# Optimization experiments

Measured on AMD Instinct MI355X. Metric: run time of the kernel, lower is better.

The kernel has to match this reference:

```python
import jax, jax.numpy as jnp
import numpy as np

B, S, L = 512, 150, 50          # batch, history length, prediction horizon
D, H, FF, NL = 128, 8, 256, 2   # d_model, heads, ffn hidden, encoder layers
DT = 0.1                        # self.dt


def _layernorm(x, g, b, eps=1e-5):
    mu = jnp.mean(x, axis=-1, keepdims=True)
    var = jnp.mean((x - mu) ** 2, axis=-1, keepdims=True)
    return (x - mu) / jnp.sqrt(var + eps) * g + b


def setup_inputs() -> dict:
    key = jax.random.key(0)
    ks = jax.random.split(key, 16)
    # inputs[:, :, :] = (position y, speed v, gap s, delta_v) over history
    pos = 100.0 * jax.random.uniform(ks[0], (B, S), jnp.float32)
    vel = 5.0 + 20.0 * jax.random.uniform(ks[1], (B, S), jnp.float32)
    gap = 10.0 + 30.0 * jax.random.uniform(ks[2], (B, S), jnp.float32)
    dvel = 0.5 * jax.random.normal(ks[3], (B, S), jnp.float32)
    inputs = jnp.stack([pos, vel, gap, dvel], axis=-1)
    # his_labels: leader position / speed over the horizon; keep leader ahead
    lead_y = inputs[:, -1, 0:1] + inputs[:, -1, 2:3] + 15.0 * jnp.arange(1, L + 1, dtype=jnp.float32)[None, :]
    lead_v = 15.0 + 2.0 * jax.random.uniform(ks[4], (B, L), jnp.float32)
    his_labels = jnp.stack([lead_y, lead_v], axis=-1)

    def u(k, shape, scale=0.05):
        return scale * jax.random.normal(k, shape, jnp.float32)

    params = dict(
        emb_w=u(ks[5], (D, 1)), emb_b=jnp.zeros((D,), jnp.float32),
        ipw=u(ks[6], (NL, 3 * D, D)), ipb=jnp.zeros((NL, 3 * D), jnp.float32),
        opw=u(ks[7], (NL, D, D)), opb=jnp.zeros((NL, D), jnp.float32),
        ln1g=jnp.ones((NL, D), jnp.float32), ln1b=jnp.zeros((NL, D), jnp.float32),
        l1w=u(ks[8], (NL, FF, D)), l1b=jnp.zeros((NL, FF), jnp.float32),
        l2w=u(ks[9], (NL, D, FF)), l2b=jnp.zeros((NL, D), jnp.float32),
        ln2g=jnp.ones((NL, D), jnp.float32), ln2b=jnp.zeros((NL, D), jnp.float32),
        dec_w=u(ks[10], (1, D)), dec_b=jnp.zeros((1,), jnp.float32),
        fus_w=u(ks[11], (1, 3)), fus_b=jnp.zeros((1,), jnp.float32),
    )
    return dict(inputs=inputs, his_labels=his_labels,
                s_0_input=jnp.float32(2.0), T_input=jnp.float32(1.5),
                a_input=jnp.float32(1.0), b_input=jnp.float32(1.5),
                v_d_input=jnp.float32(30.0), **params)


def _encoder_layer(x, mask, ipw, ipb, opw, opb, ln1g, ln1b, l1w, l1b, l2w, l2b, ln2g, ln2b):
    # x: [S, B, D]; torch post-norm TransformerEncoderLayer, relu, dropout=0
    Sq, Bb, Dd = x.shape
    dh = Dd // H
    qkv = x @ ipw.T + ipb                       # [S, B, 3D]
    q, k, v = jnp.split(qkv, 3, axis=-1)

    def heads(t):                               # [S, B, D] -> [B, H, S, dh]
        return t.reshape(Sq, Bb, H, dh).transpose(1, 2, 0, 3)

    q, k, v = heads(q), heads(k), heads(v)
    scores = jnp.einsum('bhqd,bhkd->bhqk', q, k) / jnp.sqrt(jnp.float32(dh)) + mask
    attn = jax.nn.softmax(scores, axis=-1)
    o = jnp.einsum('bhqk,bhkd->bhqd', attn, v).transpose(2, 0, 1, 3).reshape(Sq, Bb, Dd)
    o = o @ opw.T + opb
    x = _layernorm(x + o, ln1g, ln1b)
    ff = jax.nn.relu(x @ l1w.T + l1b) @ l2w.T + l2b
    return _layernorm(x + ff, ln2g, ln2b)


def _idm(inp_last, his, s0, T, a, b, vd, dt):
    # inp_last: [B, 4] = (y, v, s, delta_v); his: [B, L, 2] leader (y, v)
    y, v, s, dv = inp_last[:, 0], inp_last[:, 1], inp_last[:, 2], inp_last[:, 3]
    sq = 2.0 * jnp.sqrt(a * b)
    s_x = s0 + jnp.maximum(0.0, v * T + v * dv / sq)
    a_f = a * (1.0 - (v / vd) ** 4 - (s_x / s) ** 2)
    v0 = jnp.maximum(v + a_f * dt, 0.0)
    # NOTE: faithful to the torch source's bug: after the clipping loop the
    # loop variable i == B-1, so y_pred[:,0,0] = y + v_pred[B-1,0,0]*dt uses
    # the LAST batch element's speed for every row.
    y0 = y + v0[-1] * dt

    def step(carry, his_j):
        vj, yj = carry
        dvj = his_j[:, 1] - vj
        sj = his_j[:, 0] - yj
        sx = s0 + jnp.maximum(0.0, vj * T + vj * dvj / sq)
        acc = a * (1.0 - (vj / vd) ** 4 - (sx / sj) ** 2)
        v2 = vj + acc * dt
        v2 = jnp.where(v2 <= 0.0, 0.0, v2)
        y2 = yj + v2 * dt
        return (v2, y2), y2

    _, ys = jax.lax.scan(step, (v0, y0), his[:, :L - 1].transpose(1, 0, 2))  # ys: [L-1, B]
    y_pred = jnp.concatenate([y0[:, None], ys.T], axis=1)  # [B, L]
    return y_pred[:, :, None]


def reference(inputs, his_labels, s_0_input, T_input, a_input, b_input, v_d_input,
              emb_w, emb_b, ipw, ipb, opw, opb, ln1g, ln1b,
              l1w, l1b, l2w, l2b, ln2g, ln2b, dec_w, dec_b, fus_w, fus_b):
    src_in = inputs[:, :, 0:1]                               # [B, S, 1]
    src = src_in.transpose(1, 0, 2) @ emb_w.T + emb_b       # [S, B, D]
    mask = jnp.where(jnp.tril(jnp.ones((S, S), bool)), 0.0, -jnp.inf).astype(src.dtype)
    x = src
    for l in range(NL):
        x = _encoder_layer(x, mask, ipw[l], ipb[l], opw[l], opb[l],
                           ln1g[l], ln1b[l], l1w[l], l1b[l],
                           l2w[l], l2b[l], ln2g[l], ln2b[l])
    enc = x[-1]                                              # [B, D]
    out = jnp.broadcast_to(enc, (L, B, D)) @ dec_w.T + dec_b  # [L, B, 1]
    out = out.transpose(1, 0, 2)                             # [B, L, 1]
    # hist: per-row linspace(last, last + dv*L, L+1)[1:] == last + dv*(1..L)
    last = src_in[:, -1, 0]
    dvh = (last - src_in[:, -(1 + L), 0]) / L
    hist = (last[:, None] + dvh[:, None] * jnp.arange(1, L + 1, dtype=last.dtype))[:, :, None]
    y_idm = _idm(inputs[:, -1, :], his_labels, s_0_input, T_input,
                 a_input, b_input, v_d_input, DT)
    fusion = jnp.concatenate([out, hist, y_idm], axis=2)     # [B, L, 3]
    return fusion @ fus_w.T + fus_b                          # [B, L, 1]
```

## Files before the change

kernel.cpp:

```cpp
#include <hip/hip_runtime.h>

#define BB   512
#define SS   150
#define LL   50
#define DD   128
#define HH   8
#define DHH  16
#define FFD  256
#define NLL  2
#define MM   (SS*BB)
#define MDSZ ((size_t)MM*DD)
#define MLAST 76288

typedef unsigned short u16;
typedef __attribute__((ext_vector_type(8))) short short8;
typedef __attribute__((ext_vector_type(4))) float f32x4;

__device__ __forceinline__ float bf2f(u16 u) {
    return __uint_as_float(((unsigned int)u) << 16);
}
__device__ __forceinline__ u16 f2bf(float f) {
    unsigned int x = __float_as_uint(f);
    unsigned int r = (x + 0x7fffu + ((x >> 16) & 1u)) >> 16;
    return (u16)r;
}
__device__ __forceinline__ float ldv(const void* p, size_t i, int bf) {
    return bf ? bf2f(((const u16*)p)[i]) : ((const float*)p)[i];
}
__device__ __forceinline__ float rd_scalar(const void* p) {
    const u16* q = (const u16*)p;
    u16 lo = q[0];
    if (lo != 0) return bf2f(lo);
    return *(const float*)p;
}
__device__ __forceinline__ f32x4 mfma16(short8 a, short8 b, f32x4 c) {
    return __builtin_amdgcn_mfma_f32_16x16x32_bf16(a, b, c, 0, 0, 0);
}
__device__ __forceinline__ float fexp2(float x) {
#if __has_builtin(__builtin_amdgcn_exp2f)
    return __builtin_amdgcn_exp2f(x);
#else
    return exp2f(x);
#endif
}
__device__ __forceinline__ float frcp(float x) {
#if __has_builtin(__builtin_amdgcn_rcpf)
    return __builtin_amdgcn_rcpf(x);
#else
    return 1.f / x;
#endif
}

__global__ void detect_kernel(const u16* __restrict__ ln1g, int* __restrict__ flag)
{
    *flag = (ln1g[0] == 0x3F80) ? 1 : 0;
}

#define WOFF_IPW 0
#define WOFF_OPW 98304
#define WOFF_L1W 131072
#define WOFF_L2W 196608
#define WTOTAL   262144
__global__ __launch_bounds__(256) void prep_kernel(
    const void* __restrict__ ipw, const void* __restrict__ opw,
    const void* __restrict__ l1w, const void* __restrict__ l2w,
    u16* __restrict__ wbf, const int* __restrict__ flag)
{
    int bf = *flag;
    int idx = blockIdx.x * 256 + threadIdx.x;
    if (idx >= WTOTAL) return;
    const void* src; size_t i;
    if (idx < WOFF_OPW)      { src = ipw; i = idx; }
    else if (idx < WOFF_L1W) { src = opw; i = idx - WOFF_OPW; }
    else if (idx < WOFF_L2W) { src = l1w; i = idx - WOFF_L1W; }
    else                     { src = l2w; i = idx - WOFF_L2W; }
    wbf[idx] = bf ? ((const u16*)src)[i] : f2bf(((const float*)src)[i]);
}

__global__ void prep2_kernel(
    const void* __restrict__ ipw, const void* __restrict__ ipb,
    const void* __restrict__ emb_w, const void* __restrict__ emb_b,
    float* __restrict__ uw, const int* __restrict__ flag)
{
    int bf = *flag;
    int c = threadIdx.x;
    float su = 0.f, sw = 0.f;
    for (int k = 0; k < DD; ++k) {
        float wv = ldv(ipw, (size_t)c * DD + k, bf);
        su += wv * ldv(emb_w, k, bf);
        sw += wv * ldv(emb_b, k, bf);
    }
    uw[c]       = su;
    uw[384 + c] = sw + ldv(ipb, c, bf);
}

__global__ __launch_bounds__(192) void attn0_kernel(
    const void* __restrict__ inputs, const float* __restrict__ uw,
    u16* __restrict__ o, const int* __restrict__ flag)
{
    __shared__ float pos_s[SS];
    __shared__ float pmax_s[SS];
    __shared__ float pmin_s[SS];

    int bid = blockIdx.x;
    int h = bid & 7, b = bid >> 3;
    int tid = threadIdx.x;
    int bf = *flag;

    if (tid < SS) pos_s[tid] = ldv(inputs, (size_t)(b * SS + tid) * 4 + 0, bf);
    __syncthreads();
    if (tid == 0) {
        float mx = pos_s[0], mn = pos_s[0];
        pmax_s[0] = mx; pmin_s[0] = mn;
        for (int t = 1; t < SS; ++t) {
            mx = fmaxf(mx, pos_s[t]); mn = fminf(mn, pos_s[t]);
            pmax_s[t] = mx; pmin_s[t] = mn;
        }
    }

    const float* uq = uw + h * 16;
    const float* wq = uw + 384 + h * 16;
    const float* uk = uw + 128 + h * 16;
    float A = 0.f, Bc = 0.f;
#pragma unroll
    for (int d = 0; d < 16; ++d) { A += uq[d] * uk[d]; Bc += wq[d] * uk[d]; }
    __syncthreads();

    int q = tid;
    if (q >= SS) return;
    float pq  = pos_s[q];
    const float L2E = 1.4426950408889634f;
    float cql = 0.25f * (pq * A + Bc) * L2E;
    float Ml  = fmaxf(cql * pmax_s[q], cql * pmin_s[q]);
    float s = 0.f, wsum = 0.f;
    for (int t = 0; t <= q; ++t) {
        float pt = pos_s[t];
        float e = fexp2(__builtin_fmaf(cql, pt, -Ml));
        s += e; wsum += e * pt;
    }
    float mq = wsum * frcp(s);

    const float* uv = uw + 256 + h * 16;
    const float* wv = uw + 384 + 256 + h * 16;
    u16 ov[16];
#pragma unroll
    for (int d = 0; d < 16; ++d) ov[d] = f2bf(mq * uv[d] + wv[d]);
    u16* dst = o + ((size_t)q * BB + b) * DD + h * DHH;
    *(uint4*)(dst)     = *(uint4*)(ov);
    *(uint4*)(dst + 8) = *(uint4*)(ov + 8);
}

#define LDPK 72
template<int EPI>
__global__ __launch_bounds__(256) void mfma_gemm(
    const u16* __restrict__ A, const u16* __restrict__ W,
    const void* __restrict__ bias, size_t boff,
    void* __restrict__ out, const u16* __restrict__ resid,
    int N, int K, const int* __restrict__ flag,
    const void* __restrict__ lng, const void* __restrict__ lnb, size_t goff,
    const void* __restrict__ ew, const void* __restrict__ eb)
{
    __shared__ __attribute__((aligned(16))) u16 As[64 * LDPK];
    __shared__ __attribute__((aligned(16))) u16 Bs[128 * LDPK];

    int bf = *flag;
    int tid  = threadIdx.x;
    int wave = tid >> 6, lane = tid & 63;
    int wy = wave >> 1, wx = wave & 1;
    int quad = lane >> 4, lr = lane & 15;
    int m0 = blockIdx.x * 64, n0 = blockIdx.y * 128;

    int aR = tid >> 2,          aC = (tid & 3) * 16;
    int bR0 = tid >> 2,         bC0 = (tid & 3) * 16;
    int bR1 = (tid + 256) >> 2, bC1 = (tid & 3) * 16;

    f32x4 acc[2][4] = {};

    for (int k0 = 0; k0 < K; k0 += 64) {
        const u16* ap  = A + (size_t)(m0 + aR) * K + k0 + aC;
        const u16* wp0 = W + (size_t)(n0 + bR0) * K + k0 + bC0;
        const u16* wp1 = W + (size_t)(n0 + bR1) * K + k0 + bC1;
        uint4 av0 = *(const uint4*)(ap);
        uint4 av1 = *(const uint4*)(ap + 8);
        uint4 w00 = *(const uint4*)(wp0);
        uint4 w01 = *(const uint4*)(wp0 + 8);
        uint4 w10 = *(const uint4*)(wp1);
        uint4 w11 = *(const uint4*)(wp1 + 8);
        __syncthreads();
        *(uint4*)(As + aR * LDPK + aC)       = av0;
        *(uint4*)(As + aR * LDPK + aC + 8)   = av1;
        *(uint4*)(Bs + bR0 * LDPK + bC0)     = w00;
        *(uint4*)(Bs + bR0 * LDPK + bC0 + 8) = w01;
        *(uint4*)(Bs + bR1 * LDPK + bC1)     = w10;
        *(uint4*)(Bs + bR1 * LDPK + bC1 + 8) = w11;
        __syncthreads();

#pragma unroll
        for (int ks = 0; ks < 64; ks += 32) {
            short8 a[2], b[4];
#pragma unroll
            for (int i = 0; i < 2; ++i)
                a[i] = *(const short8*)(As + (wy * 32 + i * 16 + lr) * LDPK + ks + quad * 8);
#pragma unroll
            for (int j = 0; j < 4; ++j)
                b[j] = *(const short8*)(Bs + (wx * 64 + j * 16 + lr) * LDPK + ks + quad * 8);
#pragma unroll
            for (int i = 0; i < 2; ++i)
#pragma unroll
                for (int j = 0; j < 4; ++j)
                    acc[i][j] = mfma16(a[i], b[j], acc[i][j]);
        }
    }

    if (EPI == 3 || EPI == 4) {
        float bvj[4];
#pragma unroll
        for (int j = 0; j < 4; ++j) bvj[j] = ldv(bias, boff + wx * 64 + j * 16 + lr, bf);

        float ewj[4], ebj[4], posr[2][4];
        if (EPI == 4) {
            int sblk  = m0 >> 9;
            int bbase = m0 & 511;
#pragma unroll
            for (int j = 0; j < 4; ++j) {
                int c = wx * 64 + j * 16 + lr;
                ewj[j] = ldv(ew, c, bf);
                ebj[j] = ldv(eb, c, bf);
            }
#pragma unroll
            for (int i = 0; i < 2; ++i)
#pragma unroll
                for (int r = 0; r < 4; ++r) {
                    int b = bbase + wy * 32 + i * 16 + quad * 4 + r;
                    posr[i][r] = ldv((const void*)resid, (size_t)(b * SS + sblk) * 4 + 0, bf);
                }
        }

        float s1[2][4] = {}, s2[2][4] = {};
#pragma unroll
        for (int j = 0; j < 4; ++j) {
            int c = wx * 64 + j * 16 + lr;
#pragma unroll
            for (int i = 0; i < 2; ++i)
#pragma unroll
                for (int r = 0; r < 4; ++r) {
                    int m = m0 + wy * 32 + i * 16 + quad * 4 + r;
                    float rv = (EPI == 4)
                               ? __builtin_fmaf(posr[i][r], ewj[j], ebj[j])
                               : bf2f(resid[(size_t)m * 128 + c]);
                    float v = acc[i][j][r] + bvj[j] + rv;
                    acc[i][j][r] = v;
                    s1[i][r] += v;
                    s2[i][r] += v * v;
                }
        }
#pragma unroll
        for (int i = 0; i < 2; ++i)
#pragma unroll
            for (int r = 0; r < 4; ++r)
#pragma unroll
                for (int msk = 1; msk < 16; msk <<= 1) {
                    s1[i][r] += __shfl_xor(s1[i][r], msk);
                    s2[i][r] += __shfl_xor(s2[i][r], msk);
                }

        __syncthreads();
        float* red = (float*)As;
        if (lr == 0) {
#pragma unroll
            for (int i = 0; i < 2; ++i)
#pragma unroll
                for (int r = 0; r < 4; ++r) {
                    int row = wy * 32 + i * 16 + quad * 4 + r;
                    red[wx * 128 + row]      = s1[i][r];
                    red[wx * 128 + 64 + row] = s2[i][r];
                }
        }
        __syncthreads();

        float gj[4], bj[4];
#pragma unroll
        for (int j = 0; j < 4; ++j) {
            int c = wx * 64 + j * 16 + lr;
            gj[j] = ldv(lng, goff + c, bf);
            bj[j] = ldv(lnb, goff + c, bf);
        }
#pragma unroll
        for (int i = 0; i < 2; ++i)
#pragma unroll
            for (int r = 0; r < 4; ++r) {
                int row = wy * 32 + i * 16 + quad * 4 + r;
                float t1 = red[row] + red[128 + row];
                float t2 = red[64 + row] + red[192 + row];
                float mu = t1 * (1.f / 128.f);
                float rstd = rsqrtf(t2 * (1.f / 128.f) - mu * mu + 1e-5f);
                size_t m = (size_t)(m0 + row);
#pragma unroll
                for (int j = 0; j < 4; ++j) {
                    int c = wx * 64 + j * 16 + lr;
                    ((u16*)out)[m * 128 + c] =
                        f2bf((acc[i][j][r] - mu) * rstd * gj[j] + bj[j]);
                }
            }
        return;
    }

#pragma unroll
    for (int j = 0; j < 4; ++j) {
        int c = n0 + wx * 64 + j * 16 + lr;
        float bvj = ldv(bias, boff + c, bf);
#pragma unroll
        for (int i = 0; i < 2; ++i) {
#pragma unroll
            for (int r = 0; r < 4; ++r) {
                int m = m0 + wy * 32 + i * 16 + quad * 4 + r;
                float v = acc[i][j][r] + bvj;
                if (EPI == 1) v = fmaxf(v, 0.f);
                ((u16*)out)[(size_t)m * N + c] = f2bf(v);
            }
        }
    }
}

__global__ __launch_bounds__(256) void attn1_kernel(
    const u16* __restrict__ bx, const u16* __restrict__ w1,
    const void* __restrict__ ipb, u16* __restrict__ o1, const int* __restrict__ flag)
{
    __shared__ __attribute__((aligned(16))) u16 X[SS * 128];
    __shared__ float qv[128];
    __shared__ float qt[8][132];
    __shared__ float cb_s[8];
    __shared__ float E[SS][8];
    __shared__ float ssum[8];

    int bf = *flag;
    int b = blockIdx.x;
    int tid = threadIdx.x;

    for (int idx = tid; idx < SS * 16; idx += 256) {
        int row = idx >> 4, ch = idx & 15;
        *(uint4*)(X + row * 128 + ch * 8) =
            *(const uint4*)(bx + ((size_t)(row * 512 + b)) * 128 + ch * 8);
    }
    __syncthreads();

    if (tid < 128) {
        const u16* wr = w1 + (size_t)tid * 128;
        float acc = 0.f;
        for (int kc = 0; kc < 16; ++kc) {
            short8 wv = *(const short8*)(wr + kc * 8);
            short8 xv = *(const short8*)(X + 149 * 128 + kc * 8);
#pragma unroll
            for (int i = 0; i < 8; ++i)
                acc = __builtin_fmaf(bf2f((u16)wv[i]), bf2f((u16)xv[i]), acc);
        }
        qv[tid] = acc + ldv(ipb, 384 + tid, bf);
    }
    __syncthreads();

    for (int o = tid; o < 1024; o += 256) {
        int h = o >> 7, k = o & 127;
        float acc = 0.f;
#pragma unroll
        for (int d = 0; d < 16; ++d)
            acc = __builtin_fmaf(bf2f(w1[(size_t)(128 + h * 16 + d) * 128 + k]),
                                 qv[h * 16 + d], acc);
        qt[h][k] = acc;
    }
    if (tid < 8) {
        float acc = 0.f;
#pragma unroll
        for (int d = 0; d < 16; ++d)
            acc = __builtin_fmaf(qv[tid * 16 + d],
                                 ldv(ipb, 384 + 128 + tid * 16 + d, bf), acc);
        cb_s[tid] = acc;
    }
    __syncthreads();

    const float Cs = 0.36067376022224085f;
    for (int o = tid; o < SS * 8; o += 256) {
        int t = o >> 3, h = o & 7;
        float acc = 0.f;
        for (int kc = 0; kc < 16; ++kc) {
            short8 xv = *(const short8*)(X + t * 128 + kc * 8);
#pragma unroll
            for (int i = 0; i < 8; ++i)
                acc = __builtin_fmaf(qt[h][kc * 8 + i], bf2f((u16)xv[i]), acc);
        }
        E[t][h] = fexp2((acc + cb_s[h]) * Cs);
    }
    __syncthreads();

    if (tid < 128) {
        int h = tid >> 4, j = tid & 15;
        float acc = 0.f;
        for (int t = j; t < SS; t += 16) acc += E[t][h];
#pragma unroll
        for (int m = 1; m < 16; m <<= 1) acc += __shfl_xor(acc, m);
        if (j == 0) ssum[h] = acc;
    }
    __syncthreads();

    if (tid < 128) {
        int h = tid >> 4, k0 = (tid & 15) * 8;
        float wacc[8] = {};
        for (int t = 0; t < SS; ++t) {
            float e = E[t][h];
            short8 xv = *(const short8*)(X + t * 128 + k0);
#pragma unroll
            for (int i = 0; i < 8; ++i)
                wacc[i] = __builtin_fmaf(e, bf2f((u16)xv[i]), wacc[i]);
        }
#pragma unroll
        for (int i = 0; i < 8; ++i) qt[h][k0 + i] = wacc[i];
    }
    __syncthreads();

    if (tid < 128) {
        int h = tid >> 4;
        const u16* wr = w1 + (size_t)(256 + tid) * 128;
        float acc = 0.f;
        for (int kc = 0; kc < 16; ++kc) {
            short8 wv = *(const short8*)(wr + kc * 8);
#pragma unroll
            for (int i = 0; i < 8; ++i)
                acc = __builtin_fmaf(bf2f((u16)wv[i]), qt[h][kc * 8 + i], acc);
        }
        o1[(size_t)b * 128 + tid] =
            f2bf(acc * frcp(ssum[tid >> 4]) + ldv(ipb, 384 + 256 + tid, bf));
    }
}

__global__ __launch_bounds__(64) void head_kernel(
    const u16* __restrict__ xlast, const void* __restrict__ inputs,
    const void* __restrict__ his,
    const void* s0p, const void* Tp, const void* ap, const void* bp, const void* vdp,
    const void* __restrict__ dec_w, const void* dec_b,
    const void* fus_w, const void* fus_b,
    void* __restrict__ out, const int* __restrict__ flag)
{
    int bf = *flag;
    int b = blockIdx.x * 64 + threadIdx.x;
    if (b >= BB) return;

    const u16* enc = xlast + (size_t)b * DD;
    float dot = 0.f;
    for (int d = 0; d < DD; ++d) dot += bf2f(enc[d]) * ldv(dec_w, d, bf);
    float outv = dot + ldv(dec_b, 0, bf);

    float last = ldv(inputs, (size_t)(b * SS + (SS - 1)) * 4 + 0, bf);
    float prev = ldv(inputs, (size_t)(b * SS + (SS - 1 - LL)) * 4 + 0, bf);
    float dvh = (last - prev) * (1.f / (float)LL);

    float s0 = rd_scalar(s0p), T = rd_scalar(Tp), a = rd_scalar(ap);
    float bb = rd_scalar(bp), vd = rd_scalar(vdp);
    float sq = 2.f * sqrtf(a * bb);
    const float dt = 0.1f;

    auto v0compute = [&](int bi) {
        size_t ip = (size_t)(bi * SS + (SS - 1)) * 4;
        float v  = ldv(inputs, ip + 1, bf);
        float s  = ldv(inputs, ip + 2, bf);
        float dv = ldv(inputs, ip + 3, bf);
        float sx = s0 + fmaxf(0.f, v * T + v * dv / sq);
        float r = v / vd, r2 = r * r;
        float rs = sx / s;
        float af = a * (1.f - r2 * r2 - rs * rs);
        return fmaxf(v + af * dt, 0.f);
    };
    float v0_last = v0compute(BB - 1);
    float v0      = v0compute(b);
    float y0 = last + v0_last * dt;

    float fw0 = ldv(fus_w, 0, bf), fw1 = ldv(fus_w, 1, bf), fw2 = ldv(fus_w, 2, bf);
    float fb  = ldv(fus_b, 0, bf);

    auto store = [&](int idx, float val) {
        if (bf) ((u16*)out)[idx] = f2bf(val);
        else    ((float*)out)[idx] = val;
    };

    store(b * LL + 0, fw0 * outv + fw1 * (last + dvh * 1.f) + fw2 * y0 + fb);

    float vj = v0, yj = y0;
    for (int j = 0; j < LL - 1; ++j) {
        float hy = ldv(his, (size_t)(b * LL + j) * 2 + 0, bf);
        float hv = ldv(his, (size_t)(b * LL + j) * 2 + 1, bf);
        float dvj = hv - vj;
        float sj  = hy - yj;
        float sx = s0 + fmaxf(0.f, vj * T + vj * dvj / sq);
        float r = vj / vd, r2 = r * r;
        float rs = sx / sj;
        float acc = a * (1.f - r2 * r2 - rs * rs);
        float v2 = vj + acc * dt;
        v2 = (v2 <= 0.f) ? 0.f : v2;
        float y2 = yj + v2 * dt;
        int l = j + 1;
        float histl = last + dvh * (float)(l + 1);
        store(b * LL + l, fw0 * outv + fw1 * histl + fw2 * y2 + fb);
        vj = v2; yj = y2;
    }
}

extern "C" void kernel_launch(void* const* d_in, const int* in_sizes, int n_in,
                              void* d_out, int out_size, void* d_ws, size_t ws_size,
                              hipStream_t stream)
{
    const void* inputs = d_in[0];
    const void* his    = d_in[1];
    const void* s0p    = d_in[2];
    const void* Tp     = d_in[3];
    const void* ap     = d_in[4];
    const void* bp     = d_in[5];
    const void* vdp    = d_in[6];
    const void* emb_w  = d_in[7];
    const void* emb_b  = d_in[8];
    const void* ipw    = d_in[9];
    const void* ipb    = d_in[10];
    const void* opw    = d_in[11];
    const void* opb    = d_in[12];
    const void* ln1g   = d_in[13];
    const void* ln1b   = d_in[14];
    const void* l1w    = d_in[15];
    const void* l1b    = d_in[16];
    const void* l2w    = d_in[17];
    const void* l2b    = d_in[18];
    const void* ln2g   = d_in[19];
    const void* ln2b   = d_in[20];
    const void* dec_w  = d_in[21];
    const void* dec_b  = d_in[22];
    const void* fus_w  = d_in[23];
    const void* fus_b  = d_in[24];

    u16*   wsu  = (u16*)d_ws;
    u16*   bx   = wsu;
    u16*   bo   = wsu + 4 * MDSZ;
    u16*   h1   = wsu + 5 * MDSZ;
    u16*   wbf  = wsu + 7 * MDSZ;
    int*   flag = (int*)(wsu + 7 * MDSZ + WTOTAL);
    float* uw   = (float*)(wsu + 7 * MDSZ + WTOTAL + 2);
    u16*   o1   = bo;
    u16*   y1   = bo + 512 * 128;
    u16*   z1   = bo + 2 * 512 * 128;

    detect_kernel<<<1, 1, 0, stream>>>((const u16*)ln1g, flag);
    prep_kernel<<<(WTOTAL + 255) / 256, 256, 0, stream>>>(ipw, opw, l1w, l2w, wbf, flag);
    prep2_kernel<<<1, 384, 0, stream>>>(ipw, ipb, emb_w, emb_b, uw, flag);

    attn0_kernel<<<BB * HH, 192, 0, stream>>>(inputs, uw, bo, flag);
    mfma_gemm<4><<<dim3(MM / 64, 1), 256, 0, stream>>>(
        bo, wbf + WOFF_OPW, opb, 0,
        bx, (const u16*)inputs, 128, 128, flag, ln1g, ln1b, 0,
        emb_w, emb_b);
    mfma_gemm<1><<<dim3(MM / 64, 2), 256, 0, stream>>>(
        bx, wbf + WOFF_L1W, l1b, 0,
        h1, nullptr, 256, 128, flag, nullptr, nullptr, 0,
        nullptr, nullptr);
    mfma_gemm<3><<<dim3(MM / 64, 1), 256, 0, stream>>>(
        h1, wbf + WOFF_L2W, l2b, 0,
        bx, bx, 128, 256, flag, ln2g, ln2b, 0,
        nullptr, nullptr);

    attn1_kernel<<<BB, 256, 0, stream>>>(
        bx, wbf + WOFF_IPW + (size_t)384 * 128, ipb, o1, flag);
    mfma_gemm<3><<<dim3(512 / 64, 1), 256, 0, stream>>>(
        o1, wbf + WOFF_OPW + (size_t)128 * 128, opb, 128,
        y1, bx + (size_t)MLAST * 128, 128, 128, flag, ln1g, ln1b, 128,
        nullptr, nullptr);
    mfma_gemm<1><<<dim3(512 / 64, 2), 256, 0, stream>>>(
        y1, wbf + WOFF_L1W + (size_t)256 * 128, l1b, 256,
        h1, nullptr, 256, 128, flag, nullptr, nullptr, 0,
        nullptr, nullptr);
    mfma_gemm<3><<<dim3(512 / 64, 1), 256, 0, stream>>>(
        h1, wbf + WOFF_L2W + (size_t)128 * 256, l2b, 128,
        z1, y1, 128, 256, flag, ln2g, ln2b, 128,
        nullptr, nullptr);

    head_kernel<<<BB / 64, 64, 0, stream>>>(
        z1, inputs, his, s0p, Tp, ap, bp, vdp,
        dec_w, dec_b, fus_w, fus_b, d_out, flag);

    (void)in_sizes; (void)n_in; (void)out_size; (void)ws_size;
}
```

Before: 285.8 us.

## Fold layer-0 output projection into per-head scalar coefficients, skipping the full GEMM

Layer 0's attention output is rank-limited: each head's output is an affine function of one scalar mean position. The change precomputes the out-projection weights times each head's value vector into a small table (prep3). attn0 then writes only 8 floats per token instead of a bf16 row of 128, and a new projx kernel rebuilds the pre-LayerNorm row as a 10-term sum per column plus LayerNorm. This removes the 76800x128x128 MFMA GEMM and its 128-wide intermediate write and read, in exchange for an extra tiny launch and scalar FMA work per element.

```diff
diff --git a/kernel.cpp b/kernel.cpp
--- a/kernel.cpp
+++ b/kernel.cpp
@@ -94,9 +94,32 @@
     uw[384 + c] = sw + ldv(ipb, c, bf);
 }
 
+__global__ void prep3_kernel(
+    const float* __restrict__ uw,
+    const void* __restrict__ opw, const void* __restrict__ opb,
+    const void* __restrict__ emb_w, const void* __restrict__ emb_b,
+    float* __restrict__ gbuf, const int* __restrict__ flag)
+{
+    int bf = *flag;
+    int c = threadIdx.x;
+#pragma unroll
+    for (int h = 0; h < 8; ++h) {
+        float s = 0.f;
+#pragma unroll
+        for (int d = 0; d < 16; ++d)
+            s += ldv(opw, (size_t)c * 128 + h * 16 + d, bf) * uw[256 + h * 16 + d];
+        gbuf[h * 128 + c] = s;
+    }
+    float s9 = ldv(opb, c, bf) + ldv(emb_b, c, bf);
+    for (int k = 0; k < 128; ++k)
+        s9 += ldv(opw, (size_t)c * 128 + k, bf) * uw[640 + k];
+    gbuf[9 * 128 + c] = s9;
+    gbuf[8 * 128 + c] = ldv(emb_w, c, bf);
+}
+
 __global__ __launch_bounds__(192) void attn0_kernel(
     const void* __restrict__ inputs, const float* __restrict__ uw,
-    u16* __restrict__ o, const int* __restrict__ flag)
+    float* __restrict__ coeff, const int* __restrict__ flag)
 {
     __shared__ float pos_s[SS];
     __shared__ float pmax_s[SS];
@@ -138,16 +161,60 @@
         float e = fexp2(__builtin_fmaf(cql, pt, -Ml));
         s += e; wsum += e * pt;
     }
-    float mq = wsum * frcp(s);
-
-    const float* uv = uw + 256 + h * 16;
-    const float* wv = uw + 384 + 256 + h * 16;
-    u16 ov[16];
-#pragma unroll
-    for (int d = 0; d < 16; ++d) ov[d] = f2bf(mq * uv[d] + wv[d]);
-    u16* dst = o + ((size_t)q * BB + b) * DD + h * DHH;
-    *(uint4*)(dst)     = *(uint4*)(ov);
-    *(uint4*)(dst + 8) = *(uint4*)(ov + 8);
+    coeff[(size_t)(q * 512 + b) * 8 + h] = wsum * frcp(s);
+}
+
+__global__ __launch_bounds__(256) void projx_kernel(
+    const void* __restrict__ inputs, const float* __restrict__ coeff,
+    const float* __restrict__ gbuf, u16* __restrict__ out,
+    const int* __restrict__ flag,
+    const void* __restrict__ lng, const void* __restrict__ lnb)
+{
+    __shared__ float Bs[10][128];
+    int bf = *flag;
+    int tid = threadIdx.x;
+    int m0 = blockIdx.x * 64;
+    for (int i = tid; i < 1280; i += 256) Bs[i >> 7][i & 127] = gbuf[i];
+    __syncthreads();
+
+    int row = tid >> 2, part = tid & 3;
+    int m = m0 + row;
+    int s = m >> 9, b = m & 511;
+    float pos = ldv(inputs, (size_t)(b * SS + s) * 4 + 0, bf);
+    float cf[8];
+    {
+        const f32x4* cp = (const f32x4*)(coeff + (size_t)m * 8);
+        f32x4 c0 = cp[0], c1 = cp[1];
+#pragma unroll
+        for (int i = 0; i < 4; ++i) { cf[i] = c0[i]; cf[4 + i] = c1[i]; }
+    }
+
+    int c0i = part * 32;
+    float v[32];
+    float s1 = 0.f, s2 = 0.f;
+#pragma unroll
+    for (int j = 0; j < 32; ++j) {
+        int c = c0i + j;
+        float acc = __builtin_fmaf(pos, Bs[8][c], Bs[9][c]);
+#pragma unroll
+        for (int h = 0; h < 8; ++h) acc = __builtin_fmaf(cf[h], Bs[h][c], acc);
+        v[j] = acc; s1 += acc; s2 += acc * acc;
+    }
+    s1 += __shfl_xor(s1, 1); s2 += __shfl_xor(s2, 1);
+    s1 += __shfl_xor(s1, 2); s2 += __shfl_xor(s2, 2);
+    float mu = s1 * (1.f / 128.f);
+    float rstd = rsqrtf(s2 * (1.f / 128.f) - mu * mu + 1e-5f);
+
+    u16 ov[32];
+#pragma unroll
+    for (int j = 0; j < 32; ++j) {
+        int c = c0i + j;
+        ov[j] = f2bf((v[j] - mu) * rstd * ldv(lng, c, bf) + ldv(lnb, c, bf));
+    }
+    u16* dst = out + (size_t)m * 128 + c0i;
+#pragma unroll
+    for (int j = 0; j < 32; j += 8)
+        *(uint4*)(dst + j) = *(uint4*)(ov + j);
 }
 
 #define LDPK 72
@@ -157,8 +224,7 @@
     const void* __restrict__ bias, size_t boff,
     void* __restrict__ out, const u16* __restrict__ resid,
     int N, int K, const int* __restrict__ flag,
-    const void* __restrict__ lng, const void* __restrict__ lnb, size_t goff,
-    const void* __restrict__ ew, const void* __restrict__ eb)
+    const void* __restrict__ lng, const void* __restrict__ lnb, size_t goff)
 {
     __shared__ __attribute__((aligned(16))) u16 As[64 * LDPK];
     __shared__ __attribute__((aligned(16))) u16 Bs[128 * LDPK];
@@ -212,29 +278,10 @@
         }
     }
 
-    if (EPI == 3 || EPI == 4) {
+    if (EPI == 3) {
         float bvj[4];
 #pragma unroll
         for (int j = 0; j < 4; ++j) bvj[j] = ldv(bias, boff + wx * 64 + j * 16 + lr, bf);
-
-        float ewj[4], ebj[4], posr[2][4];
-        if (EPI == 4) {
-            int sblk  = m0 >> 9;
-            int bbase = m0 & 511;
-#pragma unroll
-            for (int j = 0; j < 4; ++j) {
-                int c = wx * 64 + j * 16 + lr;
-                ewj[j] = ldv(ew, c, bf);
-                ebj[j] = ldv(eb, c, bf);
-            }
-#pragma unroll
-            for (int i = 0; i < 2; ++i)
-#pragma unroll
-                for (int r = 0; r < 4; ++r) {
-                    int b = bbase + wy * 32 + i * 16 + quad * 4 + r;
-                    posr[i][r] = ldv((const void*)resid, (size_t)(b * SS + sblk) * 4 + 0, bf);
-                }
-        }
 
         float s1[2][4] = {}, s2[2][4] = {};
 #pragma unroll
@@ -245,10 +292,8 @@
 #pragma unroll
                 for (int r = 0; r < 4; ++r) {
                     int m = m0 + wy * 32 + i * 16 + quad * 4 + r;
-                    float rv = (EPI == 4)
-                               ? __builtin_fmaf(posr[i][r], ewj[j], ebj[j])
-                               : bf2f(resid[(size_t)m * 128 + c]);
-                    float v = acc[i][j][r] + bvj[j] + rv;
+                    float v = acc[i][j][r] + bvj[j] +
+                              bf2f(resid[(size_t)m * 128 + c]);
                     acc[i][j][r] = v;
                     s1[i][r] += v;
                     s2[i][r] += v * v;
@@ -532,49 +577,44 @@
     const void* fus_w  = d_in[23];
     const void* fus_b  = d_in[24];
 
-    u16*   wsu  = (u16*)d_ws;
-    u16*   bx   = wsu;
-    u16*   bo   = wsu + 4 * MDSZ;
-    u16*   h1   = wsu + 5 * MDSZ;
-    u16*   wbf  = wsu + 7 * MDSZ;
-    int*   flag = (int*)(wsu + 7 * MDSZ + WTOTAL);
-    float* uw   = (float*)(wsu + 7 * MDSZ + WTOTAL + 2);
-    u16*   o1   = bo;
-    u16*   y1   = bo + 512 * 128;
-    u16*   z1   = bo + 2 * 512 * 128;
+    u16*   wsu   = (u16*)d_ws;
+    u16*   bx    = wsu;
+    u16*   bo    = wsu + 4 * MDSZ;
+    u16*   h1    = wsu + 5 * MDSZ;
+    u16*   wbf   = wsu + 7 * MDSZ;
+    int*   flag  = (int*)(wsu + 7 * MDSZ + WTOTAL);
+    float* uw    = (float*)(wsu + 7 * MDSZ + WTOTAL + 2);
+    float* gbuf  = (float*)(wsu + 7 * MDSZ + WTOTAL + 4096);
+    float* coeff = (float*)(wsu + 7 * MDSZ + WTOTAL + 16384);
+    u16*   o1    = bo;
+    u16*   y1    = bo + 512 * 128;
+    u16*   z1    = bo + 2 * 512 * 128;
 
     detect_kernel<<<1, 1, 0, stream>>>((const u16*)ln1g, flag);
     prep_kernel<<<(WTOTAL + 255) / 256, 256, 0, stream>>>(ipw, opw, l1w, l2w, wbf, flag);
     prep2_kernel<<<1, 384, 0, stream>>>(ipw, ipb, emb_w, emb_b, uw, flag);
-
-    attn0_kernel<<<BB * HH, 192, 0, stream>>>(inputs, uw, bo, flag);
-    mfma_gemm<4><<<dim3(MM / 64, 1), 256, 0, stream>>>(
-        bo, wbf + WOFF_OPW, opb, 0,
-        bx, (const u16*)inputs, 128, 128, flag, ln1g, ln1b, 0,
-        emb_w, emb_b);
+    prep3_kernel<<<1, 128, 0, stream>>>(uw, opw, opb, emb_w, emb_b, gbuf, flag);
+
+    attn0_kernel<<<BB * HH, 192, 0, stream>>>(inputs, uw, coeff, flag);
+    projx_kernel<<<MM / 64, 256, 0, stream>>>(inputs, coeff, gbuf, bx, flag, ln1g, ln1b);
     mfma_gemm<1><<<dim3(MM / 64, 2), 256, 0, stream>>>(
         bx, wbf + WOFF_L1W, l1b, 0,
-        h1, nullptr, 256, 128, flag, nullptr, nullptr, 0,
-        nullptr, nullptr);
+        h1, nullptr, 256, 128, flag, nullptr, nullptr, 0);
     mfma_gemm<3><<<dim3(MM / 64, 1), 256, 0, stream>>>(
         h1, wbf + WOFF_L2W, l2b, 0,
-        bx, bx, 128, 256, flag, ln2g, ln2b, 0,
-        nullptr, nullptr);
+        bx, bx, 128, 256, flag, ln2g, ln2b, 0);
 
     attn1_kernel<<<BB, 256, 0, stream>>>(
         bx, wbf + WOFF_IPW + (size_t)384 * 128, ipb, o1, flag);
     mfma_gemm<3><<<dim3(512 / 64, 1), 256, 0, stream>>>(
         o1, wbf + WOFF_OPW + (size_t)128 * 128, opb, 128,
-        y1, bx + (size_t)MLAST * 128, 128, 128, flag, ln1g, ln1b, 128,
-        nullptr, nullptr);
+        y1, bx + (size_t)MLAST * 128, 128, 128, flag, ln1g, ln1b, 128);
     mfma_gemm<1><<<dim3(512 / 64, 2), 256, 0, stream>>>(
         y1, wbf + WOFF_L1W + (size_t)256 * 128, l1b, 256,
-        h1, nullptr, 256, 128, flag, nullptr, nullptr, 0,
-        nullptr, nullptr);
+        h1, nullptr, 256, 128, flag, nullptr, nullptr, 0);
     mfma_gemm<3><<<dim3(512 / 64, 1), 256, 0, stream>>>(
         h1, wbf + WOFF_L2W + (size_t)128 * 256, l2b, 128,
-        z1, y1, 128, 256, flag, ln2g, ln2b, 128,
-        nullptr, nullptr);
+        z1, y1, 128, 256, flag, ln2g, ln2b, 128);
 
     head_kernel<<<BB / 64, 64, 0, stream>>>(
         z1, inputs, his, s0p, Tp, ap, bp, vdp,
```

Measured after the change: 314.9 us. 1.1x slower.

## Fuse layer-0 attention output expansion into out-projection GEMM A-operand

Applied to the files above, without the earlier changes.

The layer-0 attention kernel now writes only one scalar coefficient per (batch, head, query) instead of the full 16-wide bf16 attention output per head. The following out-projection GEMM gets a new A-mode that rebuilds the bf16 A fragments in registers from that coefficient and the per-head u/w vectors held in shared memory. This removes the write and re-read of a large [S*B, 128] bf16 intermediate in exchange for extra ALU work and bf16 conversions inside the GEMM inner loop. The coefficient loads are strided gathers across blocks.

```diff
diff --git a/kernel.cpp b/kernel.cpp
--- a/kernel.cpp
+++ b/kernel.cpp
@@ -11,6 +11,7 @@
 #define MM   (SS*BB)
 #define MDSZ ((size_t)MM*DD)
 #define MLAST 76288
+#define CSTR 160
 
 typedef unsigned short u16;
 typedef __attribute__((ext_vector_type(8))) short short8;
@@ -96,7 +97,7 @@
 
 __global__ __launch_bounds__(192) void attn0_kernel(
     const void* __restrict__ inputs, const float* __restrict__ uw,
-    u16* __restrict__ o, const int* __restrict__ flag)
+    float* __restrict__ coeff, const int* __restrict__ flag)
 {
     __shared__ float pos_s[SS];
     __shared__ float pmax_s[SS];
@@ -138,30 +139,23 @@
         float e = fexp2(__builtin_fmaf(cql, pt, -Ml));
         s += e; wsum += e * pt;
     }
-    float mq = wsum * frcp(s);
-
-    const float* uv = uw + 256 + h * 16;
-    const float* wv = uw + 384 + 256 + h * 16;
-    u16 ov[16];
-#pragma unroll
-    for (int d = 0; d < 16; ++d) ov[d] = f2bf(mq * uv[d] + wv[d]);
-    u16* dst = o + ((size_t)q * BB + b) * DD + h * DHH;
-    *(uint4*)(dst)     = *(uint4*)(ov);
-    *(uint4*)(dst + 8) = *(uint4*)(ov + 8);
+    coeff[(size_t)bid * CSTR + q] = wsum * frcp(s);
 }
 
 #define LDPK 72
-template<int EPI>
+template<int EPI, int AMODE>
 __global__ __launch_bounds__(256) void mfma_gemm(
     const u16* __restrict__ A, const u16* __restrict__ W,
     const void* __restrict__ bias, size_t boff,
     void* __restrict__ out, const u16* __restrict__ resid,
     int N, int K, const int* __restrict__ flag,
     const void* __restrict__ lng, const void* __restrict__ lnb, size_t goff,
-    const void* __restrict__ ew, const void* __restrict__ eb)
+    const void* __restrict__ ew, const void* __restrict__ eb,
+    const float* __restrict__ coeff, const float* __restrict__ uwp)
 {
     __shared__ __attribute__((aligned(16))) u16 As[64 * LDPK];
     __shared__ __attribute__((aligned(16))) u16 Bs[128 * LDPK];
+    __shared__ float uvL[128], wvL[128];
 
     int bf = *flag;
     int tid  = threadIdx.x;
@@ -174,21 +168,42 @@
     int bR0 = tid >> 2,         bC0 = (tid & 3) * 16;
     int bR1 = (tid + 256) >> 2, bC1 = (tid & 3) * 16;
 
+    float mqr[2][4];
+    if (AMODE == 1) {
+        if (tid < 128)      uvL[tid]       = uwp[256 + tid];
+        else if (tid < 256) wvL[tid - 128] = uwp[640 + (tid - 128)];
+        int sblk = m0 >> 9, bbase = m0 & 511;
+#pragma unroll
+        for (int i = 0; i < 2; ++i) {
+            int b = bbase + wy * 32 + i * 16 + lr;
+#pragma unroll
+            for (int j = 0; j < 4; ++j) {
+                int h = 2 * j + (quad >> 1);
+                mqr[i][j] = coeff[(size_t)(b * 8 + h) * CSTR + sblk];
+            }
+        }
+    }
+
     f32x4 acc[2][4] = {};
 
     for (int k0 = 0; k0 < K; k0 += 64) {
-        const u16* ap  = A + (size_t)(m0 + aR) * K + k0 + aC;
+        uint4 av0, av1;
+        if (AMODE == 0) {
+            const u16* ap = A + (size_t)(m0 + aR) * K + k0 + aC;
+            av0 = *(const uint4*)(ap);
+            av1 = *(const uint4*)(ap + 8);
+        }
         const u16* wp0 = W + (size_t)(n0 + bR0) * K + k0 + bC0;
         const u16* wp1 = W + (size_t)(n0 + bR1) * K + k0 + bC1;
-        uint4 av0 = *(const uint4*)(ap);
-        uint4 av1 = *(const uint4*)(ap + 8);
         uint4 w00 = *(const uint4*)(wp0);
         uint4 w01 = *(const uint4*)(wp0 + 8);
         uint4 w10 = *(const uint4*)(wp1);
         uint4 w11 = *(const uint4*)(wp1 + 8);
         __syncthreads();
-        *(uint4*)(As + aR * LDPK + aC)       = av0;
-        *(uint4*)(As + aR * LDPK + aC + 8)   = av1;
+        if (AMODE == 0) {
+            *(uint4*)(As + aR * LDPK + aC)     = av0;
+            *(uint4*)(As + aR * LDPK + aC + 8) = av1;
+        }
         *(uint4*)(Bs + bR0 * LDPK + bC0)     = w00;
         *(uint4*)(Bs + bR0 * LDPK + bC0 + 8) = w01;
         *(uint4*)(Bs + bR1 * LDPK + bC1)     = w10;
@@ -198,9 +213,22 @@
 #pragma unroll
         for (int ks = 0; ks < 64; ks += 32) {
             short8 a[2], b[4];
-#pragma unroll
-            for (int i = 0; i < 2; ++i)
-                a[i] = *(const short8*)(As + (wy * 32 + i * 16 + lr) * LDPK + ks + quad * 8);
+            if (AMODE == 0) {
+#pragma unroll
+                for (int i = 0; i < 2; ++i)
+                    a[i] = *(const short8*)(As + (wy * 32 + i * 16 + lr) * LDPK + ks + quad * 8);
+            } else {
+                int j = (k0 >> 5) + (ks >> 5);
+                int h = 2 * j + (quad >> 1);
+                int dbase = h * 16 + (quad & 1) * 8;
+#pragma unroll
+                for (int i = 0; i < 2; ++i) {
+                    float mqv = mqr[i][j];
+#pragma unroll
+                    for (int e = 0; e < 8; ++e)
+                        a[i][e] = (short)f2bf(mqv * uvL[dbase + e] + wvL[dbase + e]);
+                }
+            }
 #pragma unroll
             for (int j = 0; j < 4; ++j)
                 b[j] = *(const short8*)(Bs + (wx * 64 + j * 16 + lr) * LDPK + ks + quad * 8);
@@ -532,49 +560,50 @@
     const void* fus_w  = d_in[23];
     const void* fus_b  = d_in[24];
 
-    u16*   wsu  = (u16*)d_ws;
-    u16*   bx   = wsu;
-    u16*   bo   = wsu + 4 * MDSZ;
-    u16*   h1   = wsu + 5 * MDSZ;
-    u16*   wbf  = wsu + 7 * MDSZ;
-    int*   flag = (int*)(wsu + 7 * MDSZ + WTOTAL);
-    float* uw   = (float*)(wsu + 7 * MDSZ + WTOTAL + 2);
-    u16*   o1   = bo;
-    u16*   y1   = bo + 512 * 128;
-    u16*   z1   = bo + 2 * 512 * 128;
+    u16*   wsu   = (u16*)d_ws;
+    u16*   bx    = wsu;
+    u16*   bo    = wsu + 4 * MDSZ;
+    u16*   h1    = wsu + 5 * MDSZ;
+    u16*   wbf   = wsu + 7 * MDSZ;
+    int*   flag  = (int*)(wsu + 7 * MDSZ + WTOTAL);
+    float* uw    = (float*)(wsu + 7 * MDSZ + WTOTAL + 2);
+    float* coeff = (float*)(wsu + 7 * MDSZ + WTOTAL + 16384);
+    u16*   o1    = bo;
+    u16*   y1    = bo + 512 * 128;
+    u16*   z1    = bo + 2 * 512 * 128;
 
     detect_kernel<<<1, 1, 0, stream>>>((const u16*)ln1g, flag);
     prep_kernel<<<(WTOTAL + 255) / 256, 256, 0, stream>>>(ipw, opw, l1w, l2w, wbf, flag);
     prep2_kernel<<<1, 384, 0, stream>>>(ipw, ipb, emb_w, emb_b, uw, flag);
 
-    attn0_kernel<<<BB * HH, 192, 0, stream>>>(inputs, uw, bo, flag);
-    mfma_gemm<4><<<dim3(MM / 64, 1), 256, 0, stream>>>(
-        bo, wbf + WOFF_OPW, opb, 0,
+    attn0_kernel<<<BB * HH, 192, 0, stream>>>(inputs, uw, coeff, flag);
+    mfma_gemm<4, 1><<<dim3(MM / 64, 1), 256, 0, stream>>>(
+        nullptr, wbf + WOFF_OPW, opb, 0,
         bx, (const u16*)inputs, 128, 128, flag, ln1g, ln1b, 0,
-        emb_w, emb_b);
-    mfma_gemm<1><<<dim3(MM / 64, 2), 256, 0, stream>>>(
+        emb_w, emb_b, coeff, uw);
+    mfma_gemm<1, 0><<<dim3(MM / 64, 2), 256, 0, stream>>>(
         bx, wbf + WOFF_L1W, l1b, 0,
         h1, nullptr, 256, 128, flag, nullptr, nullptr, 0,
-        nullptr, nullptr);
-    mfma_gemm<3><<<dim3(MM / 64, 1), 256, 0, stream>>>(
+        nullptr, nullptr, nullptr, nullptr);
+    mfma_gemm<3, 0><<<dim3(MM / 64, 1), 256, 0, stream>>>(
         h1, wbf + WOFF_L2W, l2b, 0,
         bx, bx, 128, 256, flag, ln2g, ln2b, 0,
-        nullptr, nullptr);
+        nullptr, nullptr, nullptr, nullptr);
 
     attn1_kernel<<<BB, 256, 0, stream>>>(
         bx, wbf + WOFF_IPW + (size_t)384 * 128, ipb, o1, flag);
-    mfma_gemm<3><<<dim3(512 / 64, 1), 256, 0, stream>>>(
+    mfma_gemm<3, 0><<<dim3(512 / 64, 1), 256, 0, stream>>>(
         o1, wbf + WOFF_OPW + (size_t)128 * 128, opb, 128,
         y1, bx + (size_t)MLAST * 128, 128, 128, flag, ln1g, ln1b, 128,
-        nullptr, nullptr);
-    mfma_gemm<1><<<dim3(512 / 64, 2), 256, 0, stream>>>(
+        nullptr, nullptr, nullptr, nullptr);
+    mfma_gemm<1, 0><<<dim3(512 / 64, 2), 256, 0, stream>>>(
         y1, wbf + WOFF_L1W + (size_t)256 * 128, l1b, 256,
         h1, nullptr, 256, 128, flag, nullptr, nullptr, 0,
-        nullptr, nullptr);
-    mfma_gemm<3><<<dim3(512 / 64, 1), 256, 0, stream>>>(
+        nullptr, nullptr, nullptr, nullptr);
+    mfma_gemm<3, 0><<<dim3(512 / 64, 1), 256, 0, stream>>>(
         h1, wbf + WOFF_L2W + (size_t)128 * 256, l2b, 128,
         z1, y1, 128, 256, flag, ln2g, ln2b, 128,
-        nullptr, nullptr);
+        nullptr, nullptr, nullptr, nullptr);
 
     head_kernel<<<BB / 64, 64, 0, stream>>>(
         z1, inputs, his, s0p, Tp, ap, bp, vdp,
```

Result: slower. 291.7 us (+2.1%).
